# Optimization experiments

Measured on AMD Instinct MI355X. Metric: run time of the kernel, lower is better.

Reference implementation:

```python
import jax, jax.numpy as jnp
import numpy as np

BLOCK_L = 32
STRIDE = 16
DIM = 128
N_DOWN = 5  # log2(BLOCK_L)


def setup_inputs() -> dict:
    key = jax.random.key(0)
    ks = jax.random.split(key, 4)
    B, H, S, D = 2, 16, 8192, DIM
    k = jax.random.normal(ks[0], (B, H, S, D), dtype=jnp.float32)
    pe = jax.random.normal(ks[1], (BLOCK_L, D), dtype=jnp.float32)
    # torch Linear weights [out, in]; down: Linear(2*dim, dim), scaled like default init
    w_down = jax.random.normal(ks[2], (N_DOWN, D, 2 * D), dtype=jnp.float32) / jnp.sqrt(2.0 * D)
    w_stop = jax.random.normal(ks[3], (D, D), dtype=jnp.float32) / jnp.sqrt(1.0 * D)
    return {"k": k, "pe": pe, "w_down": w_down, "w_stop": w_stop}


def reference(k, pe, w_down, w_stop):
    B, H, S, D = k.shape
    L = pe.shape[0]
    nb = (S - L) // STRIDE + 1  # number of sliding windows
    # unfold(-2, L, STRIDE).mT -> [B, H, nb, L, D]
    idx = STRIDE * jnp.arange(nb)[:, None] + jnp.arange(L)[None, :]  # [nb, L]
    x = k[:, :, idx, :] + pe  # broadcast pe over [B, H, nb]
    # prepend a zero block along the window axis
    x = jnp.concatenate([jnp.zeros_like(x[:, :, :1]), x], axis=2)  # [B, H, nb+1, L, D]
    # Phi: hierarchical pairwise merge, log2(L) stages
    for i in range(N_DOWN):
        Lc = x.shape[-2]
        x = x.reshape(*x.shape[:-2], Lc // 2, 2 * D)
        x = jax.nn.silu(jnp.einsum('...i,oi->...o', x, w_down[i]))
    out = jnp.einsum('...i,oi->...o', x, w_stop)  # [B, H, nb+1, 1, D]
    return out.squeeze(-2)
```

## Files before the change

kernel.cpp:

```cpp
#include <hip/hip_runtime.h>

#define BQ 2
#define HQ 16
#define SQ 8192
#define DQ 128
#define STR 16
#define NWIN 511
#define NBLK 512
#define WPB 4
#define NWG_PER_HEAD 128

typedef float f32x4 __attribute__((ext_vector_type(4)));
typedef short s16x8 __attribute__((ext_vector_type(8)));
typedef short s16x4 __attribute__((ext_vector_type(4)));

#define R_KIN 0u
#define R_S0  20480u
#define R_S1  0u
#define R_S2  8192u
#define R_S3  12288u
#define R_S4  14336u

static __device__ __forceinline__ unsigned swz(unsigned b) {
    return b ^ (((b >> 9) & 7u) << 4);
}

static __device__ __forceinline__ short f2bf(float f) {
    __bf16 h = (__bf16)f;
    return __builtin_bit_cast(short, h);
}

static __device__ __forceinline__ float silu(float v) {
    return v * __builtin_amdgcn_rcpf(1.f + __expf(-v));
}

__global__ void prep_kernel(const float* __restrict__ wd,
                            const float* __restrict__ wstop,
                            const float* __restrict__ pe,
                            short* __restrict__ o,
                            float* __restrict__ bias,
                            float* __restrict__ out) {
    int blk = blockIdx.x;
    if (blk < 704) {
        int i = blk * 256 + threadIdx.x;
        if (i < 163840) {
            int s   = i >> 15;
            int r   = i & 32767;
            int ct  = r >> 12;
            int r2  = r & 4095;
            int kt  = r2 >> 9;
            int r3  = r2 & 511;
            int ln  = r3 >> 3;
            int e   = r3 & 7;
            int ch  = ct * 16 + (ln & 15);
            int k   = kt * 32 + (ln >> 4) * 8 + e;
            o[i] = f2bf(wd[((size_t)(s * 128 + ch)) * 256 + k]);
        } else if (i < 180224) {
            int j   = i - 163840;
            int ct  = j >> 11;
            int r2  = j & 2047;
            int kt  = r2 >> 9;
            int r3  = r2 & 511;
            int ln  = r3 >> 3;
            int e   = r3 & 7;
            int ch  = ct * 16 + (ln & 15);
            int k   = kt * 32 + (ln >> 4) * 8 + e;
            o[i] = f2bf(wstop[ch * 128 + k]);
        }
    } else if (blk < 712) {
        int oo = (blk - 704) * 256 + threadIdx.x;
        int j = oo >> 7;
        int c = oo & 127;
        const float* w  = wd + (size_t)c * 256;
        const float* p0 = pe + (2 * j) * DQ;
        const float* p1 = pe + (2 * j + 1) * DQ;
        float s = 0.f;
        #pragma unroll 4
        for (int i = 0; i < 128; ++i) s += w[i] * p0[i];
        #pragma unroll 4
        for (int i = 0; i < 128; ++i) s += w[i + 128] * p1[i];
        bias[oo] = s;
    } else {
        int i = (blk - 712) * 256 + threadIdx.x;
        int bh = i >> 7, d = i & 127;
        out[(size_t)bh * NBLK * DQ + d] = 0.f;
    }
}

__global__ __launch_bounds__(512, 8)
void fused_kernel(const float* __restrict__ kin,
                  const short* __restrict__ wdb,
                  const float* __restrict__ bias0,
                  float* __restrict__ out) {
    __shared__ __align__(16) unsigned char lds[36864];

    const int bh = blockIdx.x >> 7;
    const int w0 = (blockIdx.x & 127) * WPB;
    const int tid  = threadIdx.x;
    const int lane = tid & 63;
    const int ct   = tid >> 6;
    const int kl   = lane >> 4;
    const int nl   = lane & 15;

    const float* kb = kin + (size_t)bh * SQ * DQ;
    const short* wbase = wdb + ct * 4096 + lane * 8;

    #pragma unroll
    for (int it = 0; it < 3; ++it) {
        int task = tid + it * 512;
        if (task < 1280) {
            int rr = task >> 4;
            int c8 = task & 15;
            int srow = STR * w0 + rr;
            if (srow > SQ - 1) srow = SQ - 1;
            const float* kp = kb + (size_t)srow * DQ + c8 * 8;
            f32x4 a0 = *(const f32x4*)kp;
            f32x4 a1 = *(const f32x4*)(kp + 4);
            s16x8 v;
            v[0] = f2bf(a0[0]); v[1] = f2bf(a0[1]); v[2] = f2bf(a0[2]); v[3] = f2bf(a0[3]);
            v[4] = f2bf(a1[0]); v[5] = f2bf(a1[1]); v[6] = f2bf(a1[2]); v[7] = f2bf(a1[3]);
            *(s16x8*)(lds + swz(R_KIN + (unsigned)((rr << 8) + (c8 << 4)))) = v;
        }
    }

    const f32x4 bias = *(const f32x4*)(bias0 + nl * 128 + ct * 16 + kl * 4);
    __syncthreads();

#define K_HALF_AT(P, Q, off, accv) {                                           \
        s16x8 aa0 = *(const s16x8*)((P) + (off));                              \
        s16x8 aa1 = *(const s16x8*)((Q) + (off));                              \
        s16x8 aa2 = *(const s16x8*)((P) + (off) + 128);                        \
        s16x8 aa3 = *(const s16x8*)((Q) + (off) + 128);                        \
        accv = __builtin_amdgcn_mfma_f32_16x16x32_bf16(wfh[0], aa0, accv, 0, 0, 0); \
        accv = __builtin_amdgcn_mfma_f32_16x16x32_bf16(wfh[1], aa1, accv, 0, 0, 0); \
        accv = __builtin_amdgcn_mfma_f32_16x16x32_bf16(wfh[2], aa2, accv, 0, 0, 0); \
        accv = __builtin_amdgcn_mfma_f32_16x16x32_bf16(wfh[3], aa3, accv, 0, 0, 0); }

    {
        f32x4 acc0 = bias, acc1 = bias, acc2 = bias, acc3 = bias;
        #pragma unroll
        for (int half = 0; half < 2; ++half) {
            s16x8 wfh[4];
            #pragma unroll
            for (int kt = 0; kt < 4; ++kt)
                wfh[kt] = *(const s16x8*)(wbase + (half * 4 + kt) * 512);
            unsigned pb = swz(R_KIN + ((unsigned)(2 * nl + half) << 8) + (unsigned)(kl << 4));
            const unsigned char* P = lds + pb;
            const unsigned char* Q = lds + (pb ^ 64u);
            K_HALF_AT(P, Q, 0,     acc0);
            K_HALF_AT(P, Q, 4096,  acc1);
            K_HALF_AT(P, Q, 8192,  acc2);
            K_HALF_AT(P, Q, 12288, acc3);
        }
        #pragma unroll
        for (int n = 0; n < 4; ++n) {
            f32x4 acc = (n == 0) ? acc0 : (n == 1) ? acc1 : (n == 2) ? acc2 : acc3;
            s16x4 v;
            v[0] = f2bf(silu(acc[0])); v[1] = f2bf(silu(acc[1]));
            v[2] = f2bf(silu(acc[2])); v[3] = f2bf(silu(acc[3]));
            unsigned d = (unsigned)(n * 16 + nl);
            *(s16x4*)(lds + swz(R_S0 + (d << 8) + (unsigned)(ct * 32 + kl * 8))) = v;
        }
    }
    __syncthreads();

    {
        f32x4 acc0 = {0.f, 0.f, 0.f, 0.f};
        f32x4 acc1 = {0.f, 0.f, 0.f, 0.f};
        #pragma unroll
        for (int half = 0; half < 2; ++half) {
            s16x8 wfh[4];
            #pragma unroll
            for (int kt = 0; kt < 4; ++kt)
                wfh[kt] = *(const s16x8*)(wbase + 32768 + (half * 4 + kt) * 512);
            unsigned pb = swz(R_S0 + ((unsigned)(2 * nl + half) << 8) + (unsigned)(kl << 4));
            const unsigned char* P = lds + pb;
            const unsigned char* Q = lds + (pb ^ 64u);
            K_HALF_AT(P, Q, 0,    acc0);
            K_HALF_AT(P, Q, 8192, acc1);
        }
        #pragma unroll
        for (int n = 0; n < 2; ++n) {
            f32x4 acc = n ? acc1 : acc0;
            s16x4 v;
            v[0] = f2bf(silu(acc[0])); v[1] = f2bf(silu(acc[1]));
            v[2] = f2bf(silu(acc[2])); v[3] = f2bf(silu(acc[3]));
            unsigned d = (unsigned)(n * 16 + nl);
            *(s16x4*)(lds + swz(R_S1 + (d << 8) + (unsigned)(ct * 32 + kl * 8))) = v;
        }
    }
    __syncthreads();

    const unsigned rin[3]  = {R_S1, R_S2, R_S3};
    const unsigned rout[3] = {R_S2, R_S3, R_S4};
    #pragma unroll
    for (int s = 2; s <= 4; ++s) {
        const int outRows = 32 >> (s - 1);
        int d = nl;
        int dc = (d < outRows) ? d : outRows - 1;
        f32x4 acc0 = {0.f, 0.f, 0.f, 0.f};
        #pragma unroll
        for (int half = 0; half < 2; ++half) {
            s16x8 wfh[4];
            #pragma unroll
            for (int kt = 0; kt < 4; ++kt)
                wfh[kt] = *(const s16x8*)(wbase + s * 32768 + (half * 4 + kt) * 512);
            unsigned pb = swz(rin[s - 2] + ((unsigned)(2 * dc + half) << 8) + (unsigned)(kl << 4));
            const unsigned char* P = lds + pb;
            const unsigned char* Q = lds + (pb ^ 64u);
            K_HALF_AT(P, Q, 0, acc0);
        }
        if (d < outRows) {
            s16x4 v;
            v[0] = f2bf(silu(acc0[0])); v[1] = f2bf(silu(acc0[1]));
            v[2] = f2bf(silu(acc0[2])); v[3] = f2bf(silu(acc0[3]));
            *(s16x4*)(lds + swz(rout[s - 2] + ((unsigned)d << 8) + (unsigned)(ct * 32 + kl * 8))) = v;
        }
        __syncthreads();
    }

    {
        s16x8 wfh[4];
        #pragma unroll
        for (int kt = 0; kt < 4; ++kt)
            wfh[kt] = *(const s16x8*)(wdb + 163840 + ct * 2048 + kt * 512 + lane * 8);
        int d = nl;
        int dc = (d < WPB) ? d : WPB - 1;
        f32x4 acc = {0.f, 0.f, 0.f, 0.f};
        unsigned pb = swz(R_S4 + ((unsigned)dc << 8) + (unsigned)(kl << 4));
        const unsigned char* P = lds + pb;
        const unsigned char* Q = lds + (pb ^ 64u);
        K_HALF_AT(P, Q, 0, acc);
        int w = w0 + d;
        if (d < WPB && w < NWIN) {
            *(f32x4*)(out + ((size_t)bh * NBLK + (w + 1)) * DQ + ct * 16 + kl * 4) = acc;
        }
    }
#undef K_HALF_AT
}

extern "C" void kernel_launch(void* const* d_in, const int* in_sizes, int n_in,
                              void* d_out, int out_size, void* d_ws, size_t ws_size,
                              hipStream_t stream) {
    const float* kin   = (const float*)d_in[0];
    const float* pe    = (const float*)d_in[1];
    const float* wdown = (const float*)d_in[2];
    const float* wstop = (const float*)d_in[3];
    float* out = (float*)d_out;
    short* wbf  = (short*)d_ws;
    float* bias = (float*)((char*)d_ws + 360448);

    prep_kernel<<<728, 256, 0, stream>>>(wdown, wstop, pe, wbf, bias, out);
    fused_kernel<<<BQ * HQ * NWG_PER_HEAD, 512, 0, stream>>>(kin, wbf, bias, out);
}
```

Baseline: 91.96 us.

## Use 32x32x16 bf16 MFMA for first two merge stages with new weight layout

Rewrites merge stages 0 and 1 to use 32x32x16 bf16 MFMA instead of 16x16x32. The prep kernel packs the first two weight matrices in a new fragment layout, and later stages read from an offset base. Each wave now computes a 32-channel by 32-row tile, which should cut the instruction count and weight fragment reloads. Stage 1 runs only on half the waves (rg==0), which leaves the other waves idle, and the XOR swizzle addressing changes.

```diff
diff --git a/kernel.cpp b/kernel.cpp
--- a/kernel.cpp
+++ b/kernel.cpp
@@ -11,6 +11,7 @@
 #define NWG_PER_HEAD 128
 
 typedef float f32x4 __attribute__((ext_vector_type(4)));
+typedef float f32x16 __attribute__((ext_vector_type(16)));
 typedef short s16x8 __attribute__((ext_vector_type(8)));
 typedef short s16x4 __attribute__((ext_vector_type(4)));
 
@@ -43,9 +44,22 @@
     int blk = blockIdx.x;
     if (blk < 704) {
         int i = blk * 256 + threadIdx.x;
-        if (i < 163840) {
+        if (i < 65536) {
             int s   = i >> 15;
             int r   = i & 32767;
+            int ct  = r >> 13;
+            int r2  = r & 8191;
+            int t   = r2 >> 9;
+            int r3  = r2 & 511;
+            int ln  = r3 >> 3;
+            int e   = r3 & 7;
+            int ch  = ct * 32 + (ln & 31);
+            int k   = t * 16 + (ln >> 5) * 8 + e;
+            o[i] = f2bf(wd[((size_t)(s * 128 + ch)) * 256 + k]);
+        } else if (i < 163840) {
+            int j   = i - 65536;
+            int s   = j >> 15;
+            int r   = j & 32767;
             int ct  = r >> 12;
             int r2  = r & 4095;
             int kt  = r2 >> 9;
@@ -54,7 +68,7 @@
             int e   = r3 & 7;
             int ch  = ct * 16 + (ln & 15);
             int k   = kt * 32 + (ln >> 4) * 8 + e;
-            o[i] = f2bf(wd[((size_t)(s * 128 + ch)) * 256 + k]);
+            o[i] = f2bf(wd[((size_t)((s + 2) * 128 + ch)) * 256 + k]);
         } else if (i < 180224) {
             int j   = i - 163840;
             int ct  = j >> 11;
@@ -98,12 +112,16 @@
     const int w0 = (blockIdx.x & 127) * WPB;
     const int tid  = threadIdx.x;
     const int lane = tid & 63;
-    const int ct   = tid >> 6;
+    const int wave = tid >> 6;
     const int kl   = lane >> 4;
     const int nl   = lane & 15;
+    const int lo5  = lane & 31;
+    const int hi   = lane >> 5;
+    const int ct32 = wave & 3;
+    const int rg   = wave >> 2;
+    const int ct   = wave;
 
     const float* kb = kin + (size_t)bh * SQ * DQ;
-    const short* wbase = wdb + ct * 4096 + lane * 8;
 
     #pragma unroll
     for (int it = 0; it < 3; ++it) {
@@ -123,7 +141,78 @@
         }
     }
 
-    const f32x4 bias = *(const f32x4*)(bias0 + nl * 128 + ct * 16 + kl * 4);
+    const unsigned kxr = ((unsigned)(lo5 & 7)) << 4;
+    const unsigned kxw = ((unsigned)((lo5 >> 1) & 7)) << 4;
+    const unsigned h4  = ((unsigned)hi << 4) ^ kxr;
+    __syncthreads();
+
+    {
+        const unsigned rowb = R_KIN +
+            ((unsigned)(32 * rg + 16 * (lo5 >> 4) + 2 * (lo5 & 15)) << 8);
+        f32x16 acc;
+        #pragma unroll
+        for (int a = 0; a < 4; ++a) {
+            f32x4 b4 = *(const f32x4*)(bias0 + (lo5 & 15) * 128 + ct32 * 32 + a * 8 + hi * 4);
+            acc[4 * a + 0] = b4[0]; acc[4 * a + 1] = b4[1];
+            acc[4 * a + 2] = b4[2]; acc[4 * a + 3] = b4[3];
+        }
+        #pragma unroll
+        for (int chunk = 0; chunk < 4; ++chunk) {
+            s16x8 wf[4];
+            #pragma unroll
+            for (int q = 0; q < 4; ++q)
+                wf[q] = *(const s16x8*)(wdb + ct32 * 8192 + (chunk * 4 + q) * 512 + lane * 8);
+            #pragma unroll
+            for (int q = 0; q < 4; ++q) {
+                const int t = chunk * 4 + q;
+                unsigned addr = rowb + ((t >= 8) ? 256u : 0u)
+                              + (((unsigned)((t & 7) << 5)) ^ h4);
+                s16x8 bb = *(const s16x8*)(lds + addr);
+                acc = __builtin_amdgcn_mfma_f32_32x32x16_bf16(wf[q], bb, acc, 0, 0, 0);
+            }
+        }
+        const unsigned d = (unsigned)(rg * 32 + lo5);
+        #pragma unroll
+        for (int a = 0; a < 4; ++a) {
+            s16x4 v;
+            v[0] = f2bf(silu(acc[4 * a + 0])); v[1] = f2bf(silu(acc[4 * a + 1]));
+            v[2] = f2bf(silu(acc[4 * a + 2])); v[3] = f2bf(silu(acc[4 * a + 3]));
+            unsigned ob = R_S0 + (d << 8)
+                        + (((unsigned)(ct32 * 64 + a * 16 + hi * 8)) ^ kxw);
+            *(s16x4*)(lds + ob) = v;
+        }
+    }
+    __syncthreads();
+
+    if (rg == 0) {
+        const unsigned rowb = R_S0 + ((unsigned)(2 * lo5) << 8);
+        f32x16 acc = {};
+        #pragma unroll
+        for (int chunk = 0; chunk < 4; ++chunk) {
+            s16x8 wf[4];
+            #pragma unroll
+            for (int q = 0; q < 4; ++q)
+                wf[q] = *(const s16x8*)(wdb + 32768 + ct32 * 8192 + (chunk * 4 + q) * 512 + lane * 8);
+            #pragma unroll
+            for (int q = 0; q < 4; ++q) {
+                const int t = chunk * 4 + q;
+                unsigned addr = rowb + ((t >= 8) ? 256u : 0u)
+                              + (((unsigned)((t & 7) << 5)) ^ h4);
+                s16x8 bb = *(const s16x8*)(lds + addr);
+                acc = __builtin_amdgcn_mfma_f32_32x32x16_bf16(wf[q], bb, acc, 0, 0, 0);
+            }
+        }
+        const unsigned d = (unsigned)lo5;
+        #pragma unroll
+        for (int a = 0; a < 4; ++a) {
+            s16x4 v;
+            v[0] = f2bf(silu(acc[4 * a + 0])); v[1] = f2bf(silu(acc[4 * a + 1]));
+            v[2] = f2bf(silu(acc[4 * a + 2])); v[3] = f2bf(silu(acc[4 * a + 3]));
+            unsigned ob = R_S1 + (d << 8)
+                        + (((unsigned)(ct32 * 64 + a * 16 + hi * 8)) ^ kxw);
+            *(s16x4*)(lds + ob) = v;
+        }
+    }
     __syncthreads();
 
 #define K_HALF_AT(P, Q, off, accv) {                                           \
@@ -136,63 +225,9 @@
         accv = __builtin_amdgcn_mfma_f32_16x16x32_bf16(wfh[2], aa2, accv, 0, 0, 0); \
         accv = __builtin_amdgcn_mfma_f32_16x16x32_bf16(wfh[3], aa3, accv, 0, 0, 0); }
 
-    {
-        f32x4 acc0 = bias, acc1 = bias, acc2 = bias, acc3 = bias;
-        #pragma unroll
-        for (int half = 0; half < 2; ++half) {
-            s16x8 wfh[4];
-            #pragma unroll
-            for (int kt = 0; kt < 4; ++kt)
-                wfh[kt] = *(const s16x8*)(wbase + (half * 4 + kt) * 512);
-            unsigned pb = swz(R_KIN + ((unsigned)(2 * nl + half) << 8) + (unsigned)(kl << 4));
-            const unsigned char* P = lds + pb;
-            const unsigned char* Q = lds + (pb ^ 64u);
-            K_HALF_AT(P, Q, 0,     acc0);
-            K_HALF_AT(P, Q, 4096,  acc1);
-            K_HALF_AT(P, Q, 8192,  acc2);
-            K_HALF_AT(P, Q, 12288, acc3);
-        }
-        #pragma unroll
-        for (int n = 0; n < 4; ++n) {
-            f32x4 acc = (n == 0) ? acc0 : (n == 1) ? acc1 : (n == 2) ? acc2 : acc3;
-            s16x4 v;
-            v[0] = f2bf(silu(acc[0])); v[1] = f2bf(silu(acc[1]));
-            v[2] = f2bf(silu(acc[2])); v[3] = f2bf(silu(acc[3]));
-            unsigned d = (unsigned)(n * 16 + nl);
-            *(s16x4*)(lds + swz(R_S0 + (d << 8) + (unsigned)(ct * 32 + kl * 8))) = v;
-        }
-    }
-    __syncthreads();
-
-    {
-        f32x4 acc0 = {0.f, 0.f, 0.f, 0.f};
-        f32x4 acc1 = {0.f, 0.f, 0.f, 0.f};
-        #pragma unroll
-        for (int half = 0; half < 2; ++half) {
-            s16x8 wfh[4];
-            #pragma unroll
-            for (int kt = 0; kt < 4; ++kt)
-                wfh[kt] = *(const s16x8*)(wbase + 32768 + (half * 4 + kt) * 512);
-            unsigned pb = swz(R_S0 + ((unsigned)(2 * nl + half) << 8) + (unsigned)(kl << 4));
-            const unsigned char* P = lds + pb;
-            const unsigned char* Q = lds + (pb ^ 64u);
-            K_HALF_AT(P, Q, 0,    acc0);
-            K_HALF_AT(P, Q, 8192, acc1);
-        }
-        #pragma unroll
-        for (int n = 0; n < 2; ++n) {
-            f32x4 acc = n ? acc1 : acc0;
-            s16x4 v;
-            v[0] = f2bf(silu(acc[0])); v[1] = f2bf(silu(acc[1]));
-            v[2] = f2bf(silu(acc[2])); v[3] = f2bf(silu(acc[3]));
-            unsigned d = (unsigned)(n * 16 + nl);
-            *(s16x4*)(lds + swz(R_S1 + (d << 8) + (unsigned)(ct * 32 + kl * 8))) = v;
-        }
-    }
-    __syncthreads();
-
     const unsigned rin[3]  = {R_S1, R_S2, R_S3};
     const unsigned rout[3] = {R_S2, R_S3, R_S4};
+    const short* wb16 = wdb + 65536 + ct * 4096 + lane * 8;
     #pragma unroll
     for (int s = 2; s <= 4; ++s) {
         const int outRows = 32 >> (s - 1);
@@ -204,7 +239,7 @@
             s16x8 wfh[4];
             #pragma unroll
             for (int kt = 0; kt < 4; ++kt)
-                wfh[kt] = *(const s16x8*)(wbase + s * 32768 + (half * 4 + kt) * 512);
+                wfh[kt] = *(const s16x8*)(wb16 + (s - 2) * 32768 + (half * 4 + kt) * 512);
             unsigned pb = swz(rin[s - 2] + ((unsigned)(2 * dc + half) << 8) + (unsigned)(kl << 4));
             const unsigned char* P = lds + pb;
             const unsigned char* Q = lds + (pb ^ 64u);
```

New measurement: 101.7 us. 1.11x slower.

## Retile first two merge stages as 2x4 wave grid with 32x32 per-wave tiles

Applied to the files above, without the earlier changes.

The first two down-projection stages now split work across waves in a 2-row-group by 4-column-group grid. Each wave computes two output column tiles over a subset of rows, so each LDS activation fragment feeds two MFMAs and each weight fragment is reused across two row tiles. Per wave this cuts LDS reads and global weight loads relative to the old layout, where every wave swept all rows for a single column tile. Bias is now added in the epilogue instead of seeding the accumulators. The cost is more live accumulator and weight registers per wave, which may pressure occupancy at 512 threads.

```diff
diff --git a/kernel.cpp b/kernel.cpp
--- a/kernel.cpp
+++ b/kernel.cpp
@@ -98,12 +98,14 @@
     const int w0 = (blockIdx.x & 127) * WPB;
     const int tid  = threadIdx.x;
     const int lane = tid & 63;
-    const int ct   = tid >> 6;
+    const int wave = tid >> 6;
     const int kl   = lane >> 4;
     const int nl   = lane & 15;
+    const int rg   = wave >> 2;
+    const int cg   = wave & 3;
+    const int ct   = wave;
 
     const float* kb = kin + (size_t)bh * SQ * DQ;
-    const short* wbase = wdb + ct * 4096 + lane * 8;
 
     #pragma unroll
     for (int it = 0; it < 3; ++it) {
@@ -122,8 +124,84 @@
             *(s16x8*)(lds + swz(R_KIN + (unsigned)((rr << 8) + (c8 << 4)))) = v;
         }
     }
-
-    const f32x4 bias = *(const f32x4*)(bias0 + nl * 128 + ct * 16 + kl * 4);
+    __syncthreads();
+
+    const int ct0 = 2 * cg, ct1 = 2 * cg + 1;
+    const short* wA = wdb + ct0 * 4096 + lane * 8;
+    const short* wB = wdb + ct1 * 4096 + lane * 8;
+
+    {
+        f32x4 acc00 = {}, acc10 = {};
+        f32x4 acc01 = {}, acc11 = {};
+        unsigned pb = swz(R_KIN + ((unsigned)(32 * rg + 2 * nl) << 8) + (unsigned)(kl << 4));
+        const unsigned char* P = lds + pb;
+        const unsigned char* Q = lds + (pb ^ 64u);
+        #pragma unroll
+        for (int c = 0; c < 4; ++c) {
+            const int off = ((c & 1) << 7) + ((c >> 1) << 8);
+            s16x8 wf00 = *(const s16x8*)(wA + (2 * c) * 512);
+            s16x8 wf01 = *(const s16x8*)(wA + (2 * c + 1) * 512);
+            s16x8 wf10 = *(const s16x8*)(wB + (2 * c) * 512);
+            s16x8 wf11 = *(const s16x8*)(wB + (2 * c + 1) * 512);
+            s16x8 b0 = *(const s16x8*)(P + off);
+            s16x8 b1 = *(const s16x8*)(Q + off);
+            s16x8 b2 = *(const s16x8*)(P + off + 4096);
+            s16x8 b3 = *(const s16x8*)(Q + off + 4096);
+            acc00 = __builtin_amdgcn_mfma_f32_16x16x32_bf16(wf00, b0, acc00, 0, 0, 0);
+            acc10 = __builtin_amdgcn_mfma_f32_16x16x32_bf16(wf10, b0, acc10, 0, 0, 0);
+            acc01 = __builtin_amdgcn_mfma_f32_16x16x32_bf16(wf00, b2, acc01, 0, 0, 0);
+            acc11 = __builtin_amdgcn_mfma_f32_16x16x32_bf16(wf10, b2, acc11, 0, 0, 0);
+            acc00 = __builtin_amdgcn_mfma_f32_16x16x32_bf16(wf01, b1, acc00, 0, 0, 0);
+            acc10 = __builtin_amdgcn_mfma_f32_16x16x32_bf16(wf11, b1, acc10, 0, 0, 0);
+            acc01 = __builtin_amdgcn_mfma_f32_16x16x32_bf16(wf01, b3, acc01, 0, 0, 0);
+            acc11 = __builtin_amdgcn_mfma_f32_16x16x32_bf16(wf11, b3, acc11, 0, 0, 0);
+        }
+        const f32x4 bv0 = *(const f32x4*)(bias0 + nl * 128 + ct0 * 16 + kl * 4);
+        const f32x4 bv1 = *(const f32x4*)(bias0 + nl * 128 + ct1 * 16 + kl * 4);
+        #pragma unroll
+        for (int n = 0; n < 2; ++n) {
+            f32x4 a0 = n ? acc01 : acc00;
+            f32x4 a1 = n ? acc11 : acc10;
+            unsigned d = (unsigned)(16 * (2 * rg + n) + nl);
+            s16x4 v;
+            v[0] = f2bf(silu(a0[0] + bv0[0])); v[1] = f2bf(silu(a0[1] + bv0[1]));
+            v[2] = f2bf(silu(a0[2] + bv0[2])); v[3] = f2bf(silu(a0[3] + bv0[3]));
+            *(s16x4*)(lds + swz(R_S0 + (d << 8) + (unsigned)(ct0 * 32 + kl * 8))) = v;
+            v[0] = f2bf(silu(a1[0] + bv1[0])); v[1] = f2bf(silu(a1[1] + bv1[1]));
+            v[2] = f2bf(silu(a1[2] + bv1[2])); v[3] = f2bf(silu(a1[3] + bv1[3]));
+            *(s16x4*)(lds + swz(R_S0 + (d << 8) + (unsigned)(ct1 * 32 + kl * 8))) = v;
+        }
+    }
+    __syncthreads();
+
+    {
+        f32x4 acc0 = {}, acc1 = {};
+        unsigned pb = swz(R_S0 + ((unsigned)(32 * rg + 2 * nl) << 8) + (unsigned)(kl << 4));
+        const unsigned char* P = lds + pb;
+        const unsigned char* Q = lds + (pb ^ 64u);
+        #pragma unroll
+        for (int c = 0; c < 4; ++c) {
+            const int off = ((c & 1) << 7) + ((c >> 1) << 8);
+            s16x8 wf00 = *(const s16x8*)(wA + 32768 + (2 * c) * 512);
+            s16x8 wf01 = *(const s16x8*)(wA + 32768 + (2 * c + 1) * 512);
+            s16x8 wf10 = *(const s16x8*)(wB + 32768 + (2 * c) * 512);
+            s16x8 wf11 = *(const s16x8*)(wB + 32768 + (2 * c + 1) * 512);
+            s16x8 b0 = *(const s16x8*)(P + off);
+            s16x8 b1 = *(const s16x8*)(Q + off);
+            acc0 = __builtin_amdgcn_mfma_f32_16x16x32_bf16(wf00, b0, acc0, 0, 0, 0);
+            acc1 = __builtin_amdgcn_mfma_f32_16x16x32_bf16(wf10, b0, acc1, 0, 0, 0);
+            acc0 = __builtin_amdgcn_mfma_f32_16x16x32_bf16(wf01, b1, acc0, 0, 0, 0);
+            acc1 = __builtin_amdgcn_mfma_f32_16x16x32_bf16(wf11, b1, acc1, 0, 0, 0);
+        }
+        unsigned d = (unsigned)(16 * rg + nl);
+        s16x4 v;
+        v[0] = f2bf(silu(acc0[0])); v[1] = f2bf(silu(acc0[1]));
+        v[2] = f2bf(silu(acc0[2])); v[3] = f2bf(silu(acc0[3]));
+        *(s16x4*)(lds + swz(R_S1 + (d << 8) + (unsigned)(ct0 * 32 + kl * 8))) = v;
+        v[0] = f2bf(silu(acc1[0])); v[1] = f2bf(silu(acc1[1]));
+        v[2] = f2bf(silu(acc1[2])); v[3] = f2bf(silu(acc1[3]));
+        *(s16x4*)(lds + swz(R_S1 + (d << 8) + (unsigned)(ct1 * 32 + kl * 8))) = v;
+    }
     __syncthreads();
 
 #define K_HALF_AT(P, Q, off, accv) {                                           \
@@ -136,63 +214,9 @@
         accv = __builtin_amdgcn_mfma_f32_16x16x32_bf16(wfh[2], aa2, accv, 0, 0, 0); \
         accv = __builtin_amdgcn_mfma_f32_16x16x32_bf16(wfh[3], aa3, accv, 0, 0, 0); }
 
-    {
-        f32x4 acc0 = bias, acc1 = bias, acc2 = bias, acc3 = bias;
-        #pragma unroll
-        for (int half = 0; half < 2; ++half) {
-            s16x8 wfh[4];
-            #pragma unroll
-            for (int kt = 0; kt < 4; ++kt)
-                wfh[kt] = *(const s16x8*)(wbase + (half * 4 + kt) * 512);
-            unsigned pb = swz(R_KIN + ((unsigned)(2 * nl + half) << 8) + (unsigned)(kl << 4));
-            const unsigned char* P = lds + pb;
-            const unsigned char* Q = lds + (pb ^ 64u);
-            K_HALF_AT(P, Q, 0,     acc0);
-            K_HALF_AT(P, Q, 4096,  acc1);
-            K_HALF_AT(P, Q, 8192,  acc2);
-            K_HALF_AT(P, Q, 12288, acc3);
-        }
-        #pragma unroll
-        for (int n = 0; n < 4; ++n) {
-            f32x4 acc = (n == 0) ? acc0 : (n == 1) ? acc1 : (n == 2) ? acc2 : acc3;
-            s16x4 v;
-            v[0] = f2bf(silu(acc[0])); v[1] = f2bf(silu(acc[1]));
-            v[2] = f2bf(silu(acc[2])); v[3] = f2bf(silu(acc[3]));
-            unsigned d = (unsigned)(n * 16 + nl);
-            *(s16x4*)(lds + swz(R_S0 + (d << 8) + (unsigned)(ct * 32 + kl * 8))) = v;
-        }
-    }
-    __syncthreads();
-
-    {
-        f32x4 acc0 = {0.f, 0.f, 0.f, 0.f};
-        f32x4 acc1 = {0.f, 0.f, 0.f, 0.f};
-        #pragma unroll
-        for (int half = 0; half < 2; ++half) {
-            s16x8 wfh[4];
-            #pragma unroll
-            for (int kt = 0; kt < 4; ++kt)
-                wfh[kt] = *(const s16x8*)(wbase + 32768 + (half * 4 + kt) * 512);
-            unsigned pb = swz(R_S0 + ((unsigned)(2 * nl + half) << 8) + (unsigned)(kl << 4));
-            const unsigned char* P = lds + pb;
-            const unsigned char* Q = lds + (pb ^ 64u);
-            K_HALF_AT(P, Q, 0,    acc0);
-            K_HALF_AT(P, Q, 8192, acc1);
-        }
-        #pragma unroll
-        for (int n = 0; n < 2; ++n) {
-            f32x4 acc = n ? acc1 : acc0;
-            s16x4 v;
-            v[0] = f2bf(silu(acc[0])); v[1] = f2bf(silu(acc[1]));
-            v[2] = f2bf(silu(acc[2])); v[3] = f2bf(silu(acc[3]));
-            unsigned d = (unsigned)(n * 16 + nl);
-            *(s16x4*)(lds + swz(R_S1 + (d << 8) + (unsigned)(ct * 32 + kl * 8))) = v;
-        }
-    }
-    __syncthreads();
-
     const unsigned rin[3]  = {R_S1, R_S2, R_S3};
     const unsigned rout[3] = {R_S2, R_S3, R_S4};
+    const short* wb16 = wdb + ct * 4096 + lane * 8;
     #pragma unroll
     for (int s = 2; s <= 4; ++s) {
         const int outRows = 32 >> (s - 1);
@@ -204,7 +228,7 @@
             s16x8 wfh[4];
             #pragma unroll
             for (int kt = 0; kt < 4; ++kt)
-                wfh[kt] = *(const s16x8*)(wbase + s * 32768 + (half * 4 + kt) * 512);
+                wfh[kt] = *(const s16x8*)(wb16 + s * 32768 + (half * 4 + kt) * 512);
             unsigned pb = swz(rin[s - 2] + ((unsigned)(2 * dc + half) << 8) + (unsigned)(kl << 4));
             const unsigned char* P = lds + pb;
             const unsigned char* Q = lds + (pb ^ 64u);
```

After: 101.5 us. +10.4%, slower.

## Process eight windows per workgroup with two-chunk K staging and deeper stage tiles

Applied to the files above, without the earlier changes.

Doubles the windows handled per workgroup from 4 to 8 and halves the grid. The first merge stage now runs in two chunks, reloading the input K rows into LDS between them, and the later stages compute more output rows per MFMA tile. The aim is to amortise the per-stage weight loads and barriers over more windows and to fill MFMA tiles that were previously partly wasted. In exchange, LDS use grows to 52 KB, which lowers occupancy, and the chunked load adds extra barriers.

```diff
diff --git a/kernel.cpp b/kernel.cpp
--- a/kernel.cpp
+++ b/kernel.cpp
@@ -7,8 +7,8 @@
 #define STR 16
 #define NWIN 511
 #define NBLK 512
-#define WPB 4
-#define NWG_PER_HEAD 128
+#define WPB 8
+#define NWG_PER_HEAD 64
 
 typedef float f32x4 __attribute__((ext_vector_type(4)));
 typedef short s16x8 __attribute__((ext_vector_type(8)));
@@ -17,9 +17,9 @@
 #define R_KIN 0u
 #define R_S0  20480u
 #define R_S1  0u
-#define R_S2  8192u
-#define R_S3  12288u
-#define R_S4  14336u
+#define R_S2  20480u
+#define R_S3  0u
+#define R_S4  28672u
 
 static __device__ __forceinline__ unsigned swz(unsigned b) {
     return b ^ (((b >> 9) & 7u) << 4);
@@ -87,15 +87,15 @@
     }
 }
 
-__global__ __launch_bounds__(512, 8)
+__global__ __launch_bounds__(512, 6)
 void fused_kernel(const float* __restrict__ kin,
                   const short* __restrict__ wdb,
                   const float* __restrict__ bias0,
                   float* __restrict__ out) {
-    __shared__ __align__(16) unsigned char lds[36864];
-
-    const int bh = blockIdx.x >> 7;
-    const int w0 = (blockIdx.x & 127) * WPB;
+    __shared__ __align__(16) unsigned char lds[53248];
+
+    const int bh = blockIdx.x >> 6;
+    const int w0 = (blockIdx.x & 63) * WPB;
     const int tid  = threadIdx.x;
     const int lane = tid & 63;
     const int ct   = tid >> 6;
@@ -105,26 +105,24 @@
     const float* kb = kin + (size_t)bh * SQ * DQ;
     const short* wbase = wdb + ct * 4096 + lane * 8;
 
-    #pragma unroll
-    for (int it = 0; it < 3; ++it) {
-        int task = tid + it * 512;
-        if (task < 1280) {
-            int rr = task >> 4;
-            int c8 = task & 15;
-            int srow = STR * w0 + rr;
-            if (srow > SQ - 1) srow = SQ - 1;
-            const float* kp = kb + (size_t)srow * DQ + c8 * 8;
-            f32x4 a0 = *(const f32x4*)kp;
-            f32x4 a1 = *(const f32x4*)(kp + 4);
-            s16x8 v;
-            v[0] = f2bf(a0[0]); v[1] = f2bf(a0[1]); v[2] = f2bf(a0[2]); v[3] = f2bf(a0[3]);
-            v[4] = f2bf(a1[0]); v[5] = f2bf(a1[1]); v[6] = f2bf(a1[2]); v[7] = f2bf(a1[3]);
-            *(s16x8*)(lds + swz(R_KIN + (unsigned)((rr << 8) + (c8 << 4)))) = v;
-        }
-    }
-
-    const f32x4 bias = *(const f32x4*)(bias0 + nl * 128 + ct * 16 + kl * 4);
-    __syncthreads();
+#define LOAD_KIN(cbase) {                                                      \
+        _Pragma("unroll")                                                      \
+        for (int it = 0; it < 3; ++it) {                                       \
+            int task = tid + it * 512;                                         \
+            if (task < 1280) {                                                 \
+                int rr = task >> 4;                                            \
+                int c8 = task & 15;                                            \
+                int srow = STR * w0 + (cbase) + rr;                            \
+                if (srow > SQ - 1) srow = SQ - 1;                              \
+                const float* kp = kb + (size_t)srow * DQ + c8 * 8;             \
+                f32x4 a0 = *(const f32x4*)kp;                                  \
+                f32x4 a1 = *(const f32x4*)(kp + 4);                            \
+                s16x8 v;                                                       \
+                v[0]=f2bf(a0[0]); v[1]=f2bf(a0[1]); v[2]=f2bf(a0[2]); v[3]=f2bf(a0[3]); \
+                v[4]=f2bf(a1[0]); v[5]=f2bf(a1[1]); v[6]=f2bf(a1[2]); v[7]=f2bf(a1[3]); \
+                *(s16x8*)(lds + swz(R_KIN + (unsigned)((rr << 8) + (c8 << 4)))) = v; \
+            }                                                                  \
+        } }
 
 #define K_HALF_AT(P, Q, off, accv) {                                           \
         s16x8 aa0 = *(const s16x8*)((P) + (off));                              \
@@ -136,7 +134,25 @@
         accv = __builtin_amdgcn_mfma_f32_16x16x32_bf16(wfh[2], aa2, accv, 0, 0, 0); \
         accv = __builtin_amdgcn_mfma_f32_16x16x32_bf16(wfh[3], aa3, accv, 0, 0, 0); }
 
-    {
+#define WRITE_ROW(region, d, accv) {                                           \
+        s16x4 v;                                                               \
+        v[0] = f2bf(silu((accv)[0])); v[1] = f2bf(silu((accv)[1]));            \
+        v[2] = f2bf(silu((accv)[2])); v[3] = f2bf(silu((accv)[3]));            \
+        *(s16x4*)(lds + swz((region) + ((unsigned)(d) << 8)                    \
+                            + (unsigned)(ct * 32 + kl * 8))) = v; }
+
+    const f32x4 bias = *(const f32x4*)(bias0 + nl * 128 + ct * 16 + kl * 4);
+
+    LOAD_KIN(0);
+    __syncthreads();
+
+    #pragma unroll
+    for (int c = 0; c < 2; ++c) {
+        if (c) {
+            __syncthreads();
+            LOAD_KIN(64);
+            __syncthreads();
+        }
         f32x4 acc0 = bias, acc1 = bias, acc2 = bias, acc3 = bias;
         #pragma unroll
         for (int half = 0; half < 2; ++half) {
@@ -152,21 +168,15 @@
             K_HALF_AT(P, Q, 8192,  acc2);
             K_HALF_AT(P, Q, 12288, acc3);
         }
-        #pragma unroll
-        for (int n = 0; n < 4; ++n) {
-            f32x4 acc = (n == 0) ? acc0 : (n == 1) ? acc1 : (n == 2) ? acc2 : acc3;
-            s16x4 v;
-            v[0] = f2bf(silu(acc[0])); v[1] = f2bf(silu(acc[1]));
-            v[2] = f2bf(silu(acc[2])); v[3] = f2bf(silu(acc[3]));
-            unsigned d = (unsigned)(n * 16 + nl);
-            *(s16x4*)(lds + swz(R_S0 + (d << 8) + (unsigned)(ct * 32 + kl * 8))) = v;
-        }
-    }
-    __syncthreads();
-
-    {
-        f32x4 acc0 = {0.f, 0.f, 0.f, 0.f};
-        f32x4 acc1 = {0.f, 0.f, 0.f, 0.f};
+        WRITE_ROW(R_S0, c * 64 + nl,      acc0);
+        WRITE_ROW(R_S0, c * 64 + 16 + nl, acc1);
+        WRITE_ROW(R_S0, c * 64 + 32 + nl, acc2);
+        WRITE_ROW(R_S0, c * 64 + 48 + nl, acc3);
+    }
+    __syncthreads();
+
+    {
+        f32x4 acc0 = {}, acc1 = {}, acc2 = {}, acc3 = {};
         #pragma unroll
         for (int half = 0; half < 2; ++half) {
             s16x8 wfh[4];
@@ -176,67 +186,91 @@
             unsigned pb = swz(R_S0 + ((unsigned)(2 * nl + half) << 8) + (unsigned)(kl << 4));
             const unsigned char* P = lds + pb;
             const unsigned char* Q = lds + (pb ^ 64u);
+            K_HALF_AT(P, Q, 0,     acc0);
+            K_HALF_AT(P, Q, 8192,  acc1);
+            K_HALF_AT(P, Q, 16384, acc2);
+            K_HALF_AT(P, Q, 24576, acc3);
+        }
+        WRITE_ROW(R_S1, nl,      acc0);
+        WRITE_ROW(R_S1, 16 + nl, acc1);
+        WRITE_ROW(R_S1, 32 + nl, acc2);
+        WRITE_ROW(R_S1, 48 + nl, acc3);
+    }
+    __syncthreads();
+
+    {
+        f32x4 acc0 = {}, acc1 = {};
+        #pragma unroll
+        for (int half = 0; half < 2; ++half) {
+            s16x8 wfh[4];
+            #pragma unroll
+            for (int kt = 0; kt < 4; ++kt)
+                wfh[kt] = *(const s16x8*)(wbase + 2 * 32768 + (half * 4 + kt) * 512);
+            unsigned pb = swz(R_S1 + ((unsigned)(2 * nl + half) << 8) + (unsigned)(kl << 4));
+            const unsigned char* P = lds + pb;
+            const unsigned char* Q = lds + (pb ^ 64u);
             K_HALF_AT(P, Q, 0,    acc0);
             K_HALF_AT(P, Q, 8192, acc1);
         }
-        #pragma unroll
-        for (int n = 0; n < 2; ++n) {
-            f32x4 acc = n ? acc1 : acc0;
-            s16x4 v;
-            v[0] = f2bf(silu(acc[0])); v[1] = f2bf(silu(acc[1]));
-            v[2] = f2bf(silu(acc[2])); v[3] = f2bf(silu(acc[3]));
-            unsigned d = (unsigned)(n * 16 + nl);
-            *(s16x4*)(lds + swz(R_S1 + (d << 8) + (unsigned)(ct * 32 + kl * 8))) = v;
-        }
-    }
-    __syncthreads();
-
-    const unsigned rin[3]  = {R_S1, R_S2, R_S3};
-    const unsigned rout[3] = {R_S2, R_S3, R_S4};
-    #pragma unroll
-    for (int s = 2; s <= 4; ++s) {
-        const int outRows = 32 >> (s - 1);
-        int d = nl;
-        int dc = (d < outRows) ? d : outRows - 1;
-        f32x4 acc0 = {0.f, 0.f, 0.f, 0.f};
-        #pragma unroll
-        for (int half = 0; half < 2; ++half) {
-            s16x8 wfh[4];
-            #pragma unroll
-            for (int kt = 0; kt < 4; ++kt)
-                wfh[kt] = *(const s16x8*)(wbase + s * 32768 + (half * 4 + kt) * 512);
-            unsigned pb = swz(rin[s - 2] + ((unsigned)(2 * dc + half) << 8) + (unsigned)(kl << 4));
+        WRITE_ROW(R_S2, nl,      acc0);
+        WRITE_ROW(R_S2, 16 + nl, acc1);
+    }
+    __syncthreads();
+
+    {
+        f32x4 acc0 = {};
+        #pragma unroll
+        for (int half = 0; half < 2; ++half) {
+            s16x8 wfh[4];
+            #pragma unroll
+            for (int kt = 0; kt < 4; ++kt)
+                wfh[kt] = *(const s16x8*)(wbase + 3 * 32768 + (half * 4 + kt) * 512);
+            unsigned pb = swz(R_S2 + ((unsigned)(2 * nl + half) << 8) + (unsigned)(kl << 4));
             const unsigned char* P = lds + pb;
             const unsigned char* Q = lds + (pb ^ 64u);
             K_HALF_AT(P, Q, 0, acc0);
         }
-        if (d < outRows) {
-            s16x4 v;
-            v[0] = f2bf(silu(acc0[0])); v[1] = f2bf(silu(acc0[1]));
-            v[2] = f2bf(silu(acc0[2])); v[3] = f2bf(silu(acc0[3]));
-            *(s16x4*)(lds + swz(rout[s - 2] + ((unsigned)d << 8) + (unsigned)(ct * 32 + kl * 8))) = v;
-        }
-        __syncthreads();
-    }
+        WRITE_ROW(R_S3, nl, acc0);
+    }
+    __syncthreads();
+
+    {
+        int dc = (nl < 8) ? nl : 7;
+        f32x4 acc0 = {};
+        #pragma unroll
+        for (int half = 0; half < 2; ++half) {
+            s16x8 wfh[4];
+            #pragma unroll
+            for (int kt = 0; kt < 4; ++kt)
+                wfh[kt] = *(const s16x8*)(wbase + 4 * 32768 + (half * 4 + kt) * 512);
+            unsigned pb = swz(R_S3 + ((unsigned)(2 * dc + half) << 8) + (unsigned)(kl << 4));
+            const unsigned char* P = lds + pb;
+            const unsigned char* Q = lds + (pb ^ 64u);
+            K_HALF_AT(P, Q, 0, acc0);
+        }
+        if (nl < 8) WRITE_ROW(R_S4, nl, acc0);
+    }
+    __syncthreads();
 
     {
         s16x8 wfh[4];
         #pragma unroll
         for (int kt = 0; kt < 4; ++kt)
             wfh[kt] = *(const s16x8*)(wdb + 163840 + ct * 2048 + kt * 512 + lane * 8);
-        int d = nl;
-        int dc = (d < WPB) ? d : WPB - 1;
+        int dc = (nl < 8) ? nl : 7;
         f32x4 acc = {0.f, 0.f, 0.f, 0.f};
         unsigned pb = swz(R_S4 + ((unsigned)dc << 8) + (unsigned)(kl << 4));
         const unsigned char* P = lds + pb;
         const unsigned char* Q = lds + (pb ^ 64u);
         K_HALF_AT(P, Q, 0, acc);
-        int w = w0 + d;
-        if (d < WPB && w < NWIN) {
+        int w = w0 + nl;
+        if (nl < 8 && w < NWIN) {
             *(f32x4*)(out + ((size_t)bh * NBLK + (w + 1)) * DQ + ct * 16 + kl * 4) = acc;
         }
     }
 #undef K_HALF_AT
+#undef WRITE_ROW
+#undef LOAD_KIN
 }
 
 extern "C" void kernel_launch(void* const* d_in, const int* in_sizes, int n_in,
```

New measurement: 77.66 us. 15.5% less time.
